# Kernel tuning notes

Measured on AMD Instinct MI355X. Metric: run time of the kernel, lower is better.

The kernel has to match this reference:

```python
import jax, jax.numpy as jnp
import numpy as np

EMB = 768
HEADS = 12
HEAD_DIM = EMB // HEADS
LN_EPS = 1e-5


def _layernorm(x, g, b):
    mu = jnp.mean(x, axis=-1, keepdims=True)
    var = jnp.mean(jnp.square(x - mu), axis=-1, keepdims=True)
    return (x - mu) * jax.lax.rsqrt(var + LN_EPS) * g + b


def _att_block(x, ln_g, ln_b, w_qkv, b_qkv, w_proj, b_proj):
    # x: [b, n, e]
    B, N, E = x.shape
    h, d = HEADS, HEAD_DIM
    qkv = _layernorm(x, ln_g, ln_b) @ w_qkv.T + b_qkv          # [b, n, 3e]
    # einops 'b n (h d qkv)': last axis factors as (h, d, 3), qkv innermost
    qkv = qkv.reshape(B, N, h, d, 3)
    qkv = jnp.moveaxis(qkv, (4, 2), (0, 2))                    # [3, b, h, n, d]
    q, k, v = qkv[0], qkv[1], qkv[2]
    scale = d ** (-0.5)
    # NOTE: original code DIVIDES by scale (= multiplies by sqrt(d)) -- faithful
    scores = jnp.einsum('bhqd,bhkd->bhqk', q, k) / scale       # [b, h, n, n]
    attn = jax.nn.softmax(scores, axis=-1)
    out = jnp.einsum('bhqk,bhkd->bhqd', attn, v)               # [b, h, n, d]
    out = out.transpose(0, 2, 1, 3).reshape(B, N, E)           # [b, n, e]
    return x + out @ w_proj.T + b_proj


def setup_inputs() -> dict:
    key = jax.random.key(0)
    ks = jax.random.split(key, 8)
    B, N, E = 2, 2048, EMB
    s = E ** (-0.5)
    return {
        'modal1': jax.random.normal(ks[0], (B, N, E), jnp.float32),
        'modal2': jax.random.normal(ks[1], (B, N, E), jnp.float32),
        'ln1_g': jnp.ones((E,), jnp.float32),
        'ln1_b': jnp.zeros((E,), jnp.float32),
        'w_qkv1': jax.random.normal(ks[2], (3 * E, E), jnp.float32) * s,
        'b_qkv1': jnp.zeros((3 * E,), jnp.float32),
        'w_proj1': jax.random.normal(ks[3], (E, E), jnp.float32) * s,
        'b_proj1': jnp.zeros((E,), jnp.float32),
        'ln2_g': jnp.ones((E,), jnp.float32),
        'ln2_b': jnp.zeros((E,), jnp.float32),
        'w_qkv2': jax.random.normal(ks[4], (3 * E, E), jnp.float32) * s,
        'b_qkv2': jnp.zeros((3 * E,), jnp.float32),
        'w_proj2': jax.random.normal(ks[5], (E, E), jnp.float32) * s,
        'b_proj2': jnp.zeros((E,), jnp.float32),
    }


def reference(modal1, modal2, ln1_g, ln1_b, w_qkv1, b_qkv1, w_proj1, b_proj1,
              ln2_g, ln2_b, w_qkv2, b_qkv2, w_proj2, b_proj2):
    out1 = _att_block(modal1, ln1_g, ln1_b, w_qkv1, b_qkv1, w_proj1, b_proj1)
    out2 = _att_block(modal2, ln2_g, ln2_b, w_qkv2, b_qkv2, w_proj2, b_proj2)
    return (out1, out2)
```

## Files before the change

kernel.cpp:

```cpp
#include <hip/hip_runtime.h>
#include <hip/hip_bf16.h>


typedef unsigned short u16;
typedef unsigned int   u32;
typedef __attribute__((ext_vector_type(4))) float          floatx4;
typedef __attribute__((ext_vector_type(8))) short          shortx8;

#define EMB   768
#define SEQ   2048
#define NHEAD 12
#define HDIM  64
#define RPM   4096
#define NROW  8192
#define NUNIT 48
#define LDA   40
#define LDK   72

__device__ __forceinline__ float bf2f(u16 h) {
  union { u32 u; float f; } v; v.u = ((u32)h) << 16; return v.f;
}
__device__ __forceinline__ u16 f2bf(float f) {
  union { float f; u32 u; } v; v.f = f;
  u32 r = v.u + 0x7fffu + ((v.u >> 16) & 1u);
  return (u16)(r >> 16);
}
__device__ __forceinline__ u16 f2bf_tr(float f) {
  union { float f; u32 u; } v; v.f = f;
  return (u16)(v.u >> 16);
}
__device__ __forceinline__ float swz_max16(float v) {
  union { float f; int i; } a;
  a.f = v; a.i = __builtin_amdgcn_ds_swizzle(a.i, 0x041F); v = fmaxf(v, a.f);
  a.f = v; a.i = __builtin_amdgcn_ds_swizzle(a.i, 0x081F); v = fmaxf(v, a.f);
  a.f = v; a.i = __builtin_amdgcn_ds_swizzle(a.i, 0x101F); v = fmaxf(v, a.f);
  a.f = v; a.i = __builtin_amdgcn_ds_swizzle(a.i, 0x201F); v = fmaxf(v, a.f);
  return v;
}

__global__ __launch_bounds__(256) void prep_wq(
    const float* __restrict__ wq1, const float* __restrict__ wq2,
    u16* __restrict__ wh, u16* __restrict__ wl)
{
  int bx = blockIdx.x;
  int modal = bx / 2304, rowp = bx % 2304;
  int typ = rowp / 768, hd = rowp % 768;
  const float* W = (modal ? wq2 : wq1) + (size_t)(hd * 3 + typ) * EMB;
  size_t dst = (size_t)bx * EMB;
  int t = threadIdx.x;
  #pragma unroll
  for (int i = 0; i < 3; ++i) {
    int e = t + i * 256;
    float v = W[e];
    u16 h = f2bf(v);
    wh[dst + e] = h;
    wl[dst + e] = f2bf(v - bf2f(h));
  }
}

__global__ __launch_bounds__(256) void prep_wp(
    const float* __restrict__ wp1, const float* __restrict__ wp2,
    u16* __restrict__ wh)
{
  int bx = blockIdx.x;
  int modal = bx / 768, row = bx % 768;
  const float* W = (modal ? wp2 : wp1) + (size_t)row * EMB;
  size_t dst = (size_t)bx * EMB;
  int t = threadIdx.x;
  #pragma unroll
  for (int i = 0; i < 3; ++i) {
    int e = t + i * 256;
    wh[dst + e] = f2bf(W[e]);
  }
}

__global__ __launch_bounds__(256) void k_ln(
    const float* __restrict__ x1, const float* __restrict__ x2,
    const float* __restrict__ g1, const float* __restrict__ b1,
    const float* __restrict__ g2, const float* __restrict__ b2,
    u16* __restrict__ xn_hi, u16* __restrict__ xn_lo)
{
  int row = blockIdx.x;
  int modal = row >> 12;
  const float* x = modal ? x2 : x1;
  const float* g = modal ? g2 : g1;
  const float* bb = modal ? b2 : b1;
  int r = row & (RPM - 1);
  const float* xr = x + (size_t)r * EMB;
  int t = threadIdx.x;
  float v0 = xr[t], v1 = xr[t + 256], v2 = xr[t + 512];
  float s = v0 + v1 + v2;
  float s2 = v0 * v0 + v1 * v1 + v2 * v2;
  #pragma unroll
  for (int m = 1; m < 64; m <<= 1) { s += __shfl_xor(s, m); s2 += __shfl_xor(s2, m); }
  __shared__ float ls[4], ls2[4];
  int w = t >> 6;
  if ((t & 63) == 0) { ls[w] = s; ls2[w] = s2; }
  __syncthreads();
  s = ls[0] + ls[1] + ls[2] + ls[3];
  s2 = ls2[0] + ls2[1] + ls2[2] + ls2[3];
  float mu = s * (1.0f / EMB);
  float var = s2 * (1.0f / EMB) - mu * mu;
  float rs = rsqrtf(var + 1e-5f);
  size_t base = (size_t)row * EMB;
  float vv[3] = { v0, v1, v2 };
  #pragma unroll
  for (int i = 0; i < 3; ++i) {
    int e = t + i * 256;
    float xn = (vv[i] - mu) * rs * g[e] + bb[e];
    u16 h = f2bf(xn);
    xn_hi[base + e] = h;
    xn_lo[base + e] = f2bf(xn - bf2f(h));
  }
}

__global__ __launch_bounds__(256) void k_qkv(
    const u16* __restrict__ xn_hi, const u16* __restrict__ xn_lo,
    const u16* __restrict__ wqh, const u16* __restrict__ wql,
    const float* __restrict__ bq1, const float* __restrict__ bq2,
    u16* __restrict__ q_hi, u16* __restrict__ q_lo,
    u16* __restrict__ k_hi, u16* __restrict__ k_lo,
    u16* __restrict__ vT)
{
  int mt = blockIdx.x, ntile = blockIdx.y, modal = blockIdx.z;
  const float* BQ = modal ? bq2 : bq1;
  int typ = ntile / 6;
  int hd0 = (ntile % 6) * 128;

  __shared__ u16 As_hi[128 * LDA], As_lo[128 * LDA], Wh[128 * LDA], Wl[128 * LDA];

  int tid = threadIdx.x, lane = tid & 63, w = tid >> 6;
  int wm = (w >> 1) * 64, wn = (w & 1) * 64;
  int lc = lane & 15, lq = lane >> 4;

  floatx4 acc[4][4] = {};
  size_t arow0 = (size_t)(modal * RPM + mt * 128) * EMB;
  size_t wrow0 = (size_t)(modal * 2304 + typ * 768 + hd0) * EMB;

  int c0 = tid, c1 = tid + 256;
  int r0 = c0 >> 2, cc0 = (c0 & 3) * 8;
  int r1 = c1 >> 2, cc1 = (c1 & 3) * 8;
  size_t go0 = (size_t)r0 * EMB + cc0, go1 = (size_t)r1 * EMB + cc1;

  shortx8 pAh0, pAh1, pW0, pW1, pAl0, pAl1, pL0, pL1;
  #define QKV_LOAD(k0) do { \
    pAh0 = *(const shortx8*)(xn_hi + arow0 + go0 + (k0)); \
    pAh1 = *(const shortx8*)(xn_hi + arow0 + go1 + (k0)); \
    pW0  = *(const shortx8*)(wqh + wrow0 + go0 + (k0)); \
    pW1  = *(const shortx8*)(wqh + wrow0 + go1 + (k0)); \
    if (typ != 2) { \
      pAl0 = *(const shortx8*)(xn_lo + arow0 + go0 + (k0)); \
      pAl1 = *(const shortx8*)(xn_lo + arow0 + go1 + (k0)); \
      pL0  = *(const shortx8*)(wql + wrow0 + go0 + (k0)); \
      pL1  = *(const shortx8*)(wql + wrow0 + go1 + (k0)); \
    } } while (0)

  QKV_LOAD(0);
  for (int k0 = 0; k0 < EMB; k0 += 32) {
    *(shortx8*)&As_hi[r0 * LDA + cc0] = pAh0;
    *(shortx8*)&As_hi[r1 * LDA + cc1] = pAh1;
    *(shortx8*)&Wh[r0 * LDA + cc0]    = pW0;
    *(shortx8*)&Wh[r1 * LDA + cc1]    = pW1;
    if (typ != 2) {
      *(shortx8*)&As_lo[r0 * LDA + cc0] = pAl0;
      *(shortx8*)&As_lo[r1 * LDA + cc1] = pAl1;
      *(shortx8*)&Wl[r0 * LDA + cc0]    = pL0;
      *(shortx8*)&Wl[r1 * LDA + cc1]    = pL1;
    }
    __syncthreads();
    if (k0 + 32 < EMB) QKV_LOAD(k0 + 32);

    shortx8 ah[4], al[4], wh[4], wl[4];
    #pragma unroll
    for (int i = 0; i < 4; ++i) {
      ah[i] = *(const shortx8*)&As_hi[(wm + i * 16 + lc) * LDA + lq * 8];
      wh[i] = *(const shortx8*)&Wh[(wn + i * 16 + lc) * LDA + lq * 8];
      if (typ != 2) {
        al[i] = *(const shortx8*)&As_lo[(wm + i * 16 + lc) * LDA + lq * 8];
        wl[i] = *(const shortx8*)&Wl[(wn + i * 16 + lc) * LDA + lq * 8];
      }
    }
    #pragma unroll
    for (int i = 0; i < 4; ++i)
      #pragma unroll
      for (int jn = 0; jn < 4; ++jn) {
        acc[i][jn] = __builtin_amdgcn_mfma_f32_16x16x32_bf16(ah[i], wh[jn], acc[i][jn], 0, 0, 0);
        if (typ != 2) {
          acc[i][jn] = __builtin_amdgcn_mfma_f32_16x16x32_bf16(al[i], wh[jn], acc[i][jn], 0, 0, 0);
          acc[i][jn] = __builtin_amdgcn_mfma_f32_16x16x32_bf16(ah[i], wl[jn], acc[i][jn], 0, 0, 0);
        }
      }
    __syncthreads();
  }
  #undef QKV_LOAD

  #pragma unroll
  for (int i = 0; i < 4; ++i) {
    int mrow0 = mt * 128 + wm + i * 16 + lq * 4;
    #pragma unroll
    for (int jn = 0; jn < 4; ++jn) {
      int colp = hd0 + wn + jn * 16 + lc;
      int h = colp >> 6, d = colp & 63;
      float bias = BQ[colp * 3 + typ];
      #pragma unroll
      for (int r = 0; r < 4; ++r) {
        int mrow = mrow0 + r;
        int b = mrow >> 11, nq = mrow & (SEQ - 1);
        int uu = modal * 24 + b * 12 + h;
        float val = acc[i][jn][r] + bias;
        if (typ == 0) {
          size_t o = ((size_t)uu * SEQ + nq) * HDIM + d;
          u16 hh = f2bf(val); q_hi[o] = hh; q_lo[o] = f2bf(val - bf2f(hh));
        } else if (typ == 1) {
          size_t o = ((size_t)uu * SEQ + nq) * HDIM + d;
          u16 hh = f2bf(val); k_hi[o] = hh; k_lo[o] = f2bf(val - bf2f(hh));
        } else {
          vT[((size_t)uu * HDIM + d) * SEQ + nq] = f2bf(val);
        }
      }
    }
  }
}

__global__ __launch_bounds__(256) void k_attn(
    const u16* __restrict__ q_hi, const u16* __restrict__ q_lo,
    const u16* __restrict__ k_hi, const u16* __restrict__ k_lo,
    const u16* __restrict__ vT, u16* __restrict__ attn_out)
{
  int u = blockIdx.x, qt = blockIdx.y;
  __shared__ u16 Kh[64 * LDK], Kl[64 * LDK], Vs[64 * LDK];
  __shared__ u16 Ps[4][32 * LDK];

  int tid = threadIdx.x, lane = tid & 63, w = tid >> 6;
  int lc = lane & 15, lq = lane >> 4;
  u16* psw = &Ps[w][0];

  shortx8 qh[2][2], ql[2][2];
  #pragma unroll
  for (int mi = 0; mi < 2; ++mi) {
    size_t qb = ((size_t)u * SEQ + qt * 128 + w * 32 + mi * 16 + lc) * HDIM + lq * 8;
    qh[mi][0] = *(const shortx8*)(q_hi + qb);
    qh[mi][1] = *(const shortx8*)(q_hi + qb + 32);
    ql[mi][0] = *(const shortx8*)(q_lo + qb);
    ql[mi][1] = *(const shortx8*)(q_lo + qb + 32);
  }

  shortx8 ONES;
  #pragma unroll
  for (int j = 0; j < 8; ++j) ONES[j] = (short)0x3F80;

  floatx4 O[2][4] = {};
  floatx4 Osum[2] = {};
  float mrow[2][4];
  #pragma unroll
  for (int mi = 0; mi < 2; ++mi)
    #pragma unroll
    for (int r = 0; r < 4; ++r) mrow[mi][r] = -1e30f;
  const float Cs = 11.5415603271f;

  int c0 = tid, c1 = tid + 256;
  int r0 = c0 >> 3, cc0 = (c0 & 7) * 8;
  int r1 = c1 >> 3, cc1 = (c1 & 7) * 8;
  const u16* khp0 = k_hi + ((size_t)u * SEQ + r0) * HDIM + cc0;
  const u16* khp1 = k_hi + ((size_t)u * SEQ + r1) * HDIM + cc1;
  const u16* klp0 = k_lo + ((size_t)u * SEQ + r0) * HDIM + cc0;
  const u16* klp1 = k_lo + ((size_t)u * SEQ + r1) * HDIM + cc1;
  const u16* vp0  = vT + ((size_t)u * HDIM + r0) * SEQ + cc0;
  const u16* vp1  = vT + ((size_t)u * HDIM + r1) * SEQ + cc1;

  shortx8 p0, p1, p2, p3, p4, p5;
  #define ATT_LOAD(kc) do { \
    p0 = *(const shortx8*)(khp0 + (size_t)(kc) * HDIM); \
    p1 = *(const shortx8*)(khp1 + (size_t)(kc) * HDIM); \
    p2 = *(const shortx8*)(klp0 + (size_t)(kc) * HDIM); \
    p3 = *(const shortx8*)(klp1 + (size_t)(kc) * HDIM); \
    p4 = *(const shortx8*)(vp0 + (kc)); \
    p5 = *(const shortx8*)(vp1 + (kc)); } while (0)

  ATT_LOAD(0);
  for (int kc = 0; kc < SEQ; kc += 64) {
    *(shortx8*)&Kh[r0 * LDK + cc0] = p0;
    *(shortx8*)&Kh[r1 * LDK + cc1] = p1;
    *(shortx8*)&Kl[r0 * LDK + cc0] = p2;
    *(shortx8*)&Kl[r1 * LDK + cc1] = p3;
    *(shortx8*)&Vs[r0 * LDK + cc0] = p4;
    *(shortx8*)&Vs[r1 * LDK + cc1] = p5;
    __syncthreads();
    if (kc + 64 < SEQ) ATT_LOAD(kc + 64);

    floatx4 S[2][4] = {};
    #pragma unroll
    for (int nt = 0; nt < 4; ++nt)
      #pragma unroll
      for (int ks = 0; ks < 2; ++ks) {
        shortx8 kf = *(const shortx8*)&Kh[(nt * 16 + lc) * LDK + ks * 32 + lq * 8];
        shortx8 lf = *(const shortx8*)&Kl[(nt * 16 + lc) * LDK + ks * 32 + lq * 8];
        #pragma unroll
        for (int mi = 0; mi < 2; ++mi) {
          S[mi][nt] = __builtin_amdgcn_mfma_f32_16x16x32_bf16(qh[mi][ks], kf, S[mi][nt], 0, 0, 0);
          S[mi][nt] = __builtin_amdgcn_mfma_f32_16x16x32_bf16(ql[mi][ks], kf, S[mi][nt], 0, 0, 0);
          S[mi][nt] = __builtin_amdgcn_mfma_f32_16x16x32_bf16(qh[mi][ks], lf, S[mi][nt], 0, 0, 0);
        }
      }

    #pragma unroll
    for (int mi = 0; mi < 2; ++mi) {
      float alpha[4];
      #pragma unroll
      for (int r = 0; r < 4; ++r) {
        float mc = fmaxf(fmaxf(S[mi][0][r], S[mi][1][r]), fmaxf(S[mi][2][r], S[mi][3][r]));
        mc = swz_max16(mc);
        float mn = fmaxf(mrow[mi][r], mc * Cs);
        alpha[r] = __builtin_amdgcn_exp2f(mrow[mi][r] - mn);
        mrow[mi][r] = mn;
      }
      #pragma unroll
      for (int nt = 0; nt < 4; ++nt)
        #pragma unroll
        for (int r = 0; r < 4; ++r) {
          float e = __builtin_amdgcn_exp2f(fmaf(S[mi][nt][r], Cs, -mrow[mi][r]));
          psw[(mi * 16 + lq * 4 + r) * LDK + nt * 16 + lc] = f2bf_tr(e);
        }
      #pragma unroll
      for (int nt = 0; nt < 4; ++nt)
        #pragma unroll
        for (int r = 0; r < 4; ++r) O[mi][nt][r] *= alpha[r];
      #pragma unroll
      for (int r = 0; r < 4; ++r) Osum[mi][r] *= alpha[r];
    }

    #pragma unroll
    for (int ks = 0; ks < 2; ++ks) {
      shortx8 pf[2];
      #pragma unroll
      for (int mi = 0; mi < 2; ++mi)
        pf[mi] = *(const shortx8*)&psw[(mi * 16 + lc) * LDK + ks * 32 + lq * 8];
      #pragma unroll
      for (int nt = 0; nt < 4; ++nt) {
        shortx8 vf = *(const shortx8*)&Vs[(nt * 16 + lc) * LDK + ks * 32 + lq * 8];
        #pragma unroll
        for (int mi = 0; mi < 2; ++mi)
          O[mi][nt] = __builtin_amdgcn_mfma_f32_16x16x32_bf16(pf[mi], vf, O[mi][nt], 0, 0, 0);
      }
      #pragma unroll
      for (int mi = 0; mi < 2; ++mi)
        Osum[mi] = __builtin_amdgcn_mfma_f32_16x16x32_bf16(pf[mi], ONES, Osum[mi], 0, 0, 0);
    }
    __syncthreads();
  }
  #undef ATT_LOAD

  int modal = u / 24, b = (u / 12) & 1, h = u % 12;
  #pragma unroll
  for (int mi = 0; mi < 2; ++mi)
    #pragma unroll
    for (int r = 0; r < 4; ++r) {
      float rl = __builtin_amdgcn_rcpf(Osum[mi][r]);
      int qrow = qt * 128 + w * 32 + mi * 16 + lq * 4 + r;
      size_t ob = ((size_t)(modal * RPM + b * SEQ + qrow)) * EMB + h * 64 + lc;
      #pragma unroll
      for (int nt = 0; nt < 4; ++nt)
        attn_out[ob + nt * 16] = f2bf(O[mi][nt][r] * rl);
    }
}

__global__ __launch_bounds__(256) void k_proj(
    const u16* __restrict__ ao, const u16* __restrict__ wph,
    const float* __restrict__ x1, const float* __restrict__ x2,
    const float* __restrict__ bp1, const float* __restrict__ bp2,
    float* __restrict__ out)
{
  int mt = blockIdx.x, ntile = blockIdx.y, modal = blockIdx.z;
  const float* BP = modal ? bp2 : bp1;
  const float* x  = modal ? x2 : x1;

  __shared__ u16 As[128 * LDA], Ws[128 * LDA];
  int tid = threadIdx.x, lane = tid & 63, w = tid >> 6;
  int wm = (w >> 1) * 64, wn = (w & 1) * 64;
  int lc = lane & 15, lq = lane >> 4;

  floatx4 acc[4][4] = {};
  size_t arow0 = (size_t)(modal * RPM + mt * 128) * EMB;
  int col0 = ntile * 128;
  size_t wrow0 = (size_t)(modal * 768 + col0) * EMB;

  int c0 = tid, c1 = tid + 256;
  int r0 = c0 >> 2, cc0 = (c0 & 3) * 8;
  int r1 = c1 >> 2, cc1 = (c1 & 3) * 8;
  size_t go0 = (size_t)r0 * EMB + cc0, go1 = (size_t)r1 * EMB + cc1;

  shortx8 pA0, pA1, pW0, pW1;
  #define PROJ_LOAD(k0) do { \
    pA0 = *(const shortx8*)(ao + arow0 + go0 + (k0)); \
    pA1 = *(const shortx8*)(ao + arow0 + go1 + (k0)); \
    pW0 = *(const shortx8*)(wph + wrow0 + go0 + (k0)); \
    pW1 = *(const shortx8*)(wph + wrow0 + go1 + (k0)); } while (0)

  PROJ_LOAD(0);
  for (int k0 = 0; k0 < EMB; k0 += 32) {
    *(shortx8*)&As[r0 * LDA + cc0] = pA0;
    *(shortx8*)&As[r1 * LDA + cc1] = pA1;
    *(shortx8*)&Ws[r0 * LDA + cc0] = pW0;
    *(shortx8*)&Ws[r1 * LDA + cc1] = pW1;
    __syncthreads();
    if (k0 + 32 < EMB) PROJ_LOAD(k0 + 32);

    shortx8 af[4], wf[4];
    #pragma unroll
    for (int i = 0; i < 4; ++i) {
      af[i] = *(const shortx8*)&As[(wm + i * 16 + lc) * LDA + lq * 8];
      wf[i] = *(const shortx8*)&Ws[(wn + i * 16 + lc) * LDA + lq * 8];
    }
    #pragma unroll
    for (int i = 0; i < 4; ++i)
      #pragma unroll
      for (int jn = 0; jn < 4; ++jn)
        acc[i][jn] = __builtin_amdgcn_mfma_f32_16x16x32_bf16(af[i], wf[jn], acc[i][jn], 0, 0, 0);
    __syncthreads();
  }
  #undef PROJ_LOAD

  #pragma unroll
  for (int i = 0; i < 4; ++i) {
    int mrow0 = mt * 128 + wm + i * 16 + lq * 4;
    #pragma unroll
    for (int jn = 0; jn < 4; ++jn) {
      int col = col0 + wn + jn * 16 + lc;
      float bias = BP[col];
      #pragma unroll
      for (int r = 0; r < 4; ++r) {
        int mrow = mrow0 + r;
        float val = acc[i][jn][r] + bias + x[(size_t)mrow * EMB + col];
        out[((size_t)(modal * RPM + mrow)) * EMB + col] = val;
      }
    }
  }
}

extern "C" void kernel_launch(void* const* d_in, const int* in_sizes, int n_in,
                              void* d_out, int out_size, void* d_ws, size_t ws_size,
                              hipStream_t stream) {
  const float* modal1 = (const float*)d_in[0];
  const float* modal2 = (const float*)d_in[1];
  const float* ln1_g  = (const float*)d_in[2];
  const float* ln1_b  = (const float*)d_in[3];
  const float* w_qkv1 = (const float*)d_in[4];
  const float* b_qkv1 = (const float*)d_in[5];
  const float* w_proj1= (const float*)d_in[6];
  const float* b_proj1= (const float*)d_in[7];
  const float* ln2_g  = (const float*)d_in[8];
  const float* ln2_b  = (const float*)d_in[9];
  const float* w_qkv2 = (const float*)d_in[10];
  const float* b_qkv2 = (const float*)d_in[11];
  const float* w_proj2= (const float*)d_in[12];
  const float* b_proj2= (const float*)d_in[13];
  float* out = (float*)d_out;

  const size_t BUFE = (size_t)NROW * EMB;
  const size_t WQE  = (size_t)2 * 2304 * EMB;
  u16* xn_hi = (u16*)d_ws;
  u16* xn_lo = xn_hi + BUFE;
  u16* q_hi  = xn_lo + BUFE;
  u16* q_lo  = q_hi + BUFE;
  u16* k_hi  = q_lo + BUFE;
  u16* k_lo  = k_hi + BUFE;
  u16* vT    = k_lo + BUFE;
  u16* wq_h  = vT + BUFE;
  u16* wq_l  = wq_h + WQE;
  u16* attn  = xn_hi;
  u16* wp_h  = q_lo;

  prep_wq<<<4608, 256, 0, stream>>>(w_qkv1, w_qkv2, wq_h, wq_l);
  k_ln<<<NROW, 256, 0, stream>>>(modal1, modal2, ln1_g, ln1_b, ln2_g, ln2_b, xn_hi, xn_lo);
  dim3 g2(32, 18, 2);
  k_qkv<<<g2, 256, 0, stream>>>(xn_hi, xn_lo, wq_h, wq_l, b_qkv1, b_qkv2,
                                q_hi, q_lo, k_hi, k_lo, vT);
  dim3 g3(48, 16);
  k_attn<<<g3, 256, 0, stream>>>(q_hi, q_lo, k_hi, k_lo, vT, attn);
  prep_wp<<<1536, 256, 0, stream>>>(w_proj1, w_proj2, wp_h);
  dim3 g4(32, 6, 2);
  k_proj<<<g4, 256, 0, stream>>>(attn, wp_h, modal1, modal2, b_proj1, b_proj2, out);
}
```

Before: 428.8 us.

## Load K/V MFMA fragments directly from global memory, dropping LDS staging

```diff
diff --git a/kernel.cpp b/kernel.cpp
--- a/kernel.cpp
+++ b/kernel.cpp
@@ -228,7 +228,6 @@
     const u16* __restrict__ vT, u16* __restrict__ attn_out)
 {
   int u = blockIdx.x, qt = blockIdx.y;
-  __shared__ u16 Kh[64 * LDK], Kl[64 * LDK], Vs[64 * LDK];
   __shared__ u16 Ps[4][32 * LDK];
 
   int tid = threadIdx.x, lane = tid & 63, w = tid >> 6;
@@ -258,50 +257,29 @@
     for (int r = 0; r < 4; ++r) mrow[mi][r] = -1e30f;
   const float Cs = 11.5415603271f;
 
-  int c0 = tid, c1 = tid + 256;
-  int r0 = c0 >> 3, cc0 = (c0 & 7) * 8;
-  int r1 = c1 >> 3, cc1 = (c1 & 7) * 8;
-  const u16* khp0 = k_hi + ((size_t)u * SEQ + r0) * HDIM + cc0;
-  const u16* khp1 = k_hi + ((size_t)u * SEQ + r1) * HDIM + cc1;
-  const u16* klp0 = k_lo + ((size_t)u * SEQ + r0) * HDIM + cc0;
-  const u16* klp1 = k_lo + ((size_t)u * SEQ + r1) * HDIM + cc1;
-  const u16* vp0  = vT + ((size_t)u * HDIM + r0) * SEQ + cc0;
-  const u16* vp1  = vT + ((size_t)u * HDIM + r1) * SEQ + cc1;
-
-  shortx8 p0, p1, p2, p3, p4, p5;
-  #define ATT_LOAD(kc) do { \
-    p0 = *(const shortx8*)(khp0 + (size_t)(kc) * HDIM); \
-    p1 = *(const shortx8*)(khp1 + (size_t)(kc) * HDIM); \
-    p2 = *(const shortx8*)(klp0 + (size_t)(kc) * HDIM); \
-    p3 = *(const shortx8*)(klp1 + (size_t)(kc) * HDIM); \
-    p4 = *(const shortx8*)(vp0 + (kc)); \
-    p5 = *(const shortx8*)(vp1 + (kc)); } while (0)
-
-  ATT_LOAD(0);
+  const u16* Kh_l = k_hi + (size_t)u * SEQ * HDIM + lc * HDIM + lq * 8;
+  const u16* Kl_l = k_lo + (size_t)u * SEQ * HDIM + lc * HDIM + lq * 8;
+  const u16* Vb_l = vT   + (size_t)u * HDIM * SEQ + lc * SEQ  + lq * 8;
+
   for (int kc = 0; kc < SEQ; kc += 64) {
-    *(shortx8*)&Kh[r0 * LDK + cc0] = p0;
-    *(shortx8*)&Kh[r1 * LDK + cc1] = p1;
-    *(shortx8*)&Kl[r0 * LDK + cc0] = p2;
-    *(shortx8*)&Kl[r1 * LDK + cc1] = p3;
-    *(shortx8*)&Vs[r0 * LDK + cc0] = p4;
-    *(shortx8*)&Vs[r1 * LDK + cc1] = p5;
-    __syncthreads();
-    if (kc + 64 < SEQ) ATT_LOAD(kc + 64);
-
     floatx4 S[2][4] = {};
     #pragma unroll
-    for (int nt = 0; nt < 4; ++nt)
-      #pragma unroll
-      for (int ks = 0; ks < 2; ++ks) {
-        shortx8 kf = *(const shortx8*)&Kh[(nt * 16 + lc) * LDK + ks * 32 + lq * 8];
-        shortx8 lf = *(const shortx8*)&Kl[(nt * 16 + lc) * LDK + ks * 32 + lq * 8];
+    for (int ks = 0; ks < 2; ++ks) {
+      shortx8 kf[4], lf[4];
+      #pragma unroll
+      for (int nt = 0; nt < 4; ++nt) {
+        kf[nt] = *(const shortx8*)(Kh_l + (size_t)(kc + nt * 16) * HDIM + ks * 32);
+        lf[nt] = *(const shortx8*)(Kl_l + (size_t)(kc + nt * 16) * HDIM + ks * 32);
+      }
+      #pragma unroll
+      for (int nt = 0; nt < 4; ++nt)
         #pragma unroll
         for (int mi = 0; mi < 2; ++mi) {
-          S[mi][nt] = __builtin_amdgcn_mfma_f32_16x16x32_bf16(qh[mi][ks], kf, S[mi][nt], 0, 0, 0);
-          S[mi][nt] = __builtin_amdgcn_mfma_f32_16x16x32_bf16(ql[mi][ks], kf, S[mi][nt], 0, 0, 0);
-          S[mi][nt] = __builtin_amdgcn_mfma_f32_16x16x32_bf16(qh[mi][ks], lf, S[mi][nt], 0, 0, 0);
+          S[mi][nt] = __builtin_amdgcn_mfma_f32_16x16x32_bf16(qh[mi][ks], kf[nt], S[mi][nt], 0, 0, 0);
+          S[mi][nt] = __builtin_amdgcn_mfma_f32_16x16x32_bf16(ql[mi][ks], kf[nt], S[mi][nt], 0, 0, 0);
+          S[mi][nt] = __builtin_amdgcn_mfma_f32_16x16x32_bf16(qh[mi][ks], lf[nt], S[mi][nt], 0, 0, 0);
         }
-      }
+    }
 
     #pragma unroll
     for (int mi = 0; mi < 2; ++mi) {
@@ -331,24 +309,23 @@
 
     #pragma unroll
     for (int ks = 0; ks < 2; ++ks) {
-      shortx8 pf[2];
+      shortx8 vf[4], pf[2];
+      #pragma unroll
+      for (int nt = 0; nt < 4; ++nt)
+        vf[nt] = *(const shortx8*)(Vb_l + (size_t)(nt * 16) * SEQ + kc + ks * 32);
       #pragma unroll
       for (int mi = 0; mi < 2; ++mi)
         pf[mi] = *(const shortx8*)&psw[(mi * 16 + lc) * LDK + ks * 32 + lq * 8];
       #pragma unroll
-      for (int nt = 0; nt < 4; ++nt) {
-        shortx8 vf = *(const shortx8*)&Vs[(nt * 16 + lc) * LDK + ks * 32 + lq * 8];
+      for (int nt = 0; nt < 4; ++nt)
         #pragma unroll
         for (int mi = 0; mi < 2; ++mi)
-          O[mi][nt] = __builtin_amdgcn_mfma_f32_16x16x32_bf16(pf[mi], vf, O[mi][nt], 0, 0, 0);
-      }
+          O[mi][nt] = __builtin_amdgcn_mfma_f32_16x16x32_bf16(pf[mi], vf[nt], O[mi][nt], 0, 0, 0);
       #pragma unroll
       for (int mi = 0; mi < 2; ++mi)
         Osum[mi] = __builtin_amdgcn_mfma_f32_16x16x32_bf16(pf[mi], ONES, Osum[mi], 0, 0, 0);
     }
-    __syncthreads();
-  }
-  #undef ATT_LOAD
+  }
 
   int modal = u / 24, b = (u / 12) & 1, h = u % 12;
   #pragma unroll
```

Result: slower. 555.4 us (+29.5%).
